# Performance work log

Hardware: AMD Instinct MI355X
Metric: run time of the kernel (lower is better)

The kernel has to match this reference:

```python
import jax, jax.numpy as jnp
import numpy as np

N = 50000
E = 800000
F_IN = 128


def _gat(h, src, dst, W, a_src, a_dst, bias, heads, out_ch, concat):
    n = h.shape[0]
    z = (h @ W.T).reshape(n, heads, out_ch)              # [N,H,C]
    alpha_s = jnp.sum(z * a_src, axis=-1)                # [N,H]
    alpha_d = jnp.sum(z * a_dst, axis=-1)                # [N,H]
    logits = jax.nn.leaky_relu(alpha_s[src] + alpha_d[dst], 0.2)  # [Etot,H]
    m = jax.ops.segment_max(logits, dst, num_segments=n)
    ex = jnp.exp(logits - m[dst])
    denom = jax.ops.segment_sum(ex, dst, num_segments=n)
    w = ex / (denom[dst] + 1e-16)                        # [Etot,H]
    agg = jax.ops.segment_sum(w[:, :, None] * z[src], dst, num_segments=n)  # [N,H,C]
    if concat:
        out = agg.reshape(n, heads * out_ch)
    else:
        out = agg.mean(axis=1)
    return out + bias


def setup_inputs() -> dict:
    key = jax.random.key(0)
    ks = jax.random.split(key, 16)
    s = lambda *sh: 1.0 / np.sqrt(sh[-1])
    inp = {
        "x": jax.random.normal(ks[0], (N, F_IN), jnp.float32),
        "edge_index": jax.random.randint(ks[1], (2, E), 0, N, jnp.int64),
        # GraphConv(no_node_features=128 -> 128, aggr='add')
        "W_rel": jax.random.normal(ks[2], (128, F_IN), jnp.float32) * s(128, F_IN),
        "b_rel": jnp.zeros((128,), jnp.float32),
        "W_root": jax.random.normal(ks[3], (128, F_IN), jnp.float32) * s(128, F_IN),
        # GATConv(128 -> 8, heads=8, concat) => 64
        "W1": jax.random.normal(ks[4], (64, 128), jnp.float32) * s(64, 128),
        "a1_src": jax.random.normal(ks[5], (8, 8), jnp.float32) * 0.35,
        "a1_dst": jax.random.normal(ks[6], (8, 8), jnp.float32) * 0.35,
        "b1": jnp.zeros((64,), jnp.float32),
        # GATConv(64 -> 64, heads=1, concat=False)
        "W2": jax.random.normal(ks[7], (64, 64), jnp.float32) * s(64, 64),
        "a2_src": jax.random.normal(ks[8], (1, 64), jnp.float32) * 0.125,
        "a2_dst": jax.random.normal(ks[9], (1, 64), jnp.float32) * 0.125,
        "b2": jnp.zeros((64,), jnp.float32),
        "Wr": jax.random.normal(ks[10], (1, 64), jnp.float32) * s(1, 64),
        "br": jnp.zeros((1,), jnp.float32),
    }
    return inp


def reference(x, edge_index, W_rel, b_rel, W_root, W1, a1_src, a1_dst, b1,
              W2, a2_src, a2_dst, b2, Wr, br):
    src, dst = edge_index[0], edge_index[1]
    # GraphConv, aggr='add': W_rel @ sum_{j in N(i)} x_j + b + W_root @ x_i
    nbr = jax.ops.segment_sum(x[src], dst, num_segments=N)
    h = nbr @ W_rel.T + b_rel + x @ W_root.T
    h = jax.nn.elu(h)
    # GATConv adds self-loops by default
    loop = jnp.arange(N, dtype=edge_index.dtype)
    src2 = jnp.concatenate([src, loop])
    dst2 = jnp.concatenate([dst, loop])
    h = _gat(h, src2, dst2, W1, a1_src, a1_dst, b1, heads=8, out_ch=8, concat=True)
    h = jax.nn.elu(h)
    h = _gat(h, src2, dst2, W2, a2_src, a2_dst, b2, heads=1, out_ch=64, concat=False)
    # final 'mean' aggregation over all nodes (single graph)
    g = jnp.mean(h, axis=0, keepdims=True)               # [1,64]
    return g @ Wr.T + br                                  # [1,1]
```

## Files before the change

kernel.cpp:

```cpp
#include <hip/hip_runtime.h>
#include <hip/hip_bf16.h>
#include <math.h>

#define N_NODES 50000
#define N_EDGES 800000
#define F_IN 128
#define NBUCK 391
#define EPB 4096
#define NBB 196

typedef __attribute__((ext_vector_type(8))) short bf16x8;
typedef __attribute__((ext_vector_type(4))) float f32x4;
typedef __attribute__((ext_vector_type(2))) float f32x2;
typedef unsigned long long ull;

__device__ __forceinline__ float elu_f(float x)   { return x > 0.f ? x : expm1f(x); }
__device__ __forceinline__ float lrelu_f(float x) { return x > 0.f ? x : 0.2f * x; }
__device__ __forceinline__ int   clampN(int v)    { return v < 0 ? 0 : (v >= N_NODES ? N_NODES - 1 : v); }
__device__ __forceinline__ float bits2f(unsigned int u) { union { unsigned int u; float f; } x; x.u = u; return x.f; }
__device__ __forceinline__ float lo16(unsigned int u) { return bits2f(u << 16); }
__device__ __forceinline__ float hi16(unsigned int u) { return bits2f(u & 0xffff0000u); }
__device__ __forceinline__ float bf2f(unsigned short s) { return bits2f(((unsigned int)s) << 16); }
__device__ __forceinline__ unsigned short f2bfbits(float f) {
    __hip_bfloat16 b = __float2bfloat16(f);
    return __builtin_bit_cast(unsigned short, b);
}
__device__ __forceinline__ unsigned int pack2(float lo, float hi) {
    return ((unsigned int)f2bfbits(hi) << 16) | f2bfbits(lo);
}

__global__ __launch_bounds__(256) void k_bhist(const int* __restrict__ dst,
                                               int* __restrict__ bcount) {
    __shared__ int hist[NBUCK];
    int tid = threadIdx.x;
    for (int j = tid; j < NBUCK; j += 256) hist[j] = 0;
    __syncthreads();
    int base = blockIdx.x * EPB;
    #pragma unroll
    for (int t = 0; t < EPB / 256; ++t) {
        int e = base + t * 256 + tid;
        if (e < N_EDGES) atomicAdd(&hist[clampN(dst[e]) >> 7], 1);
    }
    __syncthreads();
    for (int j = tid; j < NBUCK; j += 256)
        if (hist[j]) atomicAdd(&bcount[j], hist[j]);
}

__global__ __launch_bounds__(512) void k_bscan(const int* __restrict__ bcount,
                                               int* __restrict__ boff,
                                               int* __restrict__ bcur) {
    __shared__ int wsum[8];
    __shared__ int wbase[8];
    int tid = threadIdx.x;
    int lane = tid & 63, wid = tid >> 6;
    int v = (tid < NBUCK) ? bcount[tid] : 0;
    int x = v;
    #pragma unroll
    for (int d = 1; d < 64; d <<= 1) {
        int t = __shfl_up(x, d, 64);
        if (lane >= d) x += t;
    }
    if (lane == 63) wsum[wid] = x;
    __syncthreads();
    if (tid == 0) {
        int b = 0;
        #pragma unroll
        for (int w = 0; w < 8; ++w) { wbase[w] = b; b += wsum[w]; }
    }
    __syncthreads();
    if (tid < NBUCK) {
        int e = wbase[wid] + x - v;
        boff[tid] = e;
        bcur[tid] = e;
    }
    if (tid == 0) boff[NBUCK] = N_EDGES;
}

__global__ __launch_bounds__(256) void k_bscatter(const int* __restrict__ src,
                                                  const int* __restrict__ dst,
                                                  int* __restrict__ bcur,
                                                  unsigned int* __restrict__ ebuf) {
    __shared__ int hist[NBUCK];
    __shared__ int hbase[NBUCK];
    int tid = threadIdx.x;
    for (int j = tid; j < NBUCK; j += 256) hist[j] = 0;
    __syncthreads();
    int base = blockIdx.x * EPB;
    unsigned int myP[EPB / 256]; int myB[EPB / 256], myR[EPB / 256];
    #pragma unroll
    for (int t = 0; t < EPB / 256; ++t) {
        int e = base + t * 256 + tid;
        if (e < N_EDGES) {
            int d = clampN(dst[e]);
            int s = clampN(src[e]);
            myP[t] = ((unsigned int)s << 7) | (unsigned int)(d & 127);
            myB[t] = d >> 7;
            myR[t] = atomicAdd(&hist[d >> 7], 1);
        } else myB[t] = -1;
    }
    __syncthreads();
    for (int j = tid; j < NBUCK; j += 256)
        if (hist[j]) hbase[j] = atomicAdd(&bcur[j], hist[j]);
    __syncthreads();
    #pragma unroll
    for (int t = 0; t < EPB / 256; ++t) {
        if (myB[t] >= 0) ebuf[hbase[myB[t]] + myR[t]] = myP[t];
    }
}

__global__ __launch_bounds__(256) void k_bfinal(const unsigned int* __restrict__ ebuf,
                                                const int* __restrict__ boff,
                                                int* __restrict__ offsets,
                                                int* __restrict__ csr) {
    __shared__ int cnt[128];
    __shared__ int cur[128];
    __shared__ int ws[4];
    int b = blockIdx.x;
    int tid = threadIdx.x;
    int node0 = b << 7;
    int k0 = boff[b], k1 = boff[b + 1];
    if (tid < 128) cnt[tid] = 0;
    __syncthreads();
    for (int k = k0 + tid; k < k1; k += 256)
        atomicAdd(&cnt[ebuf[k] & 127u], 1);
    __syncthreads();
    int lane = tid & 63;
    int v = (tid < 128) ? cnt[tid] : 0;
    int x = v;
    #pragma unroll
    for (int d = 1; d < 64; d <<= 1) {
        int t = __shfl_up(x, d, 64);
        if (lane >= d) x += t;
    }
    if (lane == 63) ws[tid >> 6] = x;
    __syncthreads();
    if (tid < 128) {
        int add = (tid >> 6) ? ws[0] : 0;
        int excl = k0 + add + x - v;
        cur[tid] = excl;
        int node = node0 + tid;
        if (node < N_NODES) offsets[node] = excl;
    }
    if (b == NBUCK - 1 && tid == 0) offsets[N_NODES] = N_EDGES;
    __syncthreads();
    for (int k = k0 + tid; k < k1; k += 256) {
        unsigned int e = ebuf[k];
        int r = atomicAdd(&cur[e & 127u], 1);
        csr[r] = (int)(e >> 7);
    }
}

#define CAST_X_IDS (N_NODES * 32)
__global__ void k_cast(const float* __restrict__ x,
                       const float* __restrict__ W_rel, const float* __restrict__ W_root,
                       const float* __restrict__ W1, const float* __restrict__ W2,
                       __hip_bfloat16* __restrict__ Abuf, unsigned int* __restrict__ x8,
                       __hip_bfloat16* __restrict__ Wc,
                       __hip_bfloat16* __restrict__ W1b, __hip_bfloat16* __restrict__ W2b) {
    int id = blockIdx.x * 256 + threadIdx.x;
    if (id < CAST_X_IDS) {
        int i = id >> 5, c4 = (id & 31) * 4;
        float4 v = *(const float4*)&x[(size_t)i * 128 + c4];
        ull p = (ull)f2bfbits(v.x) | ((ull)f2bfbits(v.y) << 16)
              | ((ull)f2bfbits(v.z) << 32) | ((ull)f2bfbits(v.w) << 48);
        *(ull*)&Abuf[(size_t)i * 256 + 128 + c4] = p;
        int t = __builtin_amdgcn_cvt_pk_fp8_f32(v.x, v.y, 0, false);
        t = __builtin_amdgcn_cvt_pk_fp8_f32(v.z, v.w, t, true);
        x8[(size_t)i * 32 + (id & 31)] = (unsigned int)t;
    } else {
        int j = id - CAST_X_IDS;
        if (j < 32768) {
            int cc = j >> 8, k = j & 255;
            float v = (k < 128) ? W_rel[cc * 128 + k] : W_root[cc * 128 + (k - 128)];
            Wc[j] = __float2bfloat16(v);
        } else if (j < 32768 + 8192) {
            W1b[j - 32768] = __float2bfloat16(W1[j - 32768]);
        } else if (j < 32768 + 8192 + 4096) {
            W2b[j - 32768 - 8192] = __float2bfloat16(W2[j - 32768 - 8192]);
        }
    }
}

__global__ __launch_bounds__(256) void k_gather(const unsigned int* __restrict__ x8,
                                                const int* __restrict__ offsets,
                                                const int* __restrict__ csr,
                                                ull* __restrict__ outNbr) {
    int i = blockIdx.x * 8 + (threadIdx.x >> 5);
    int l = threadIdx.x & 31;
    int k0 = offsets[i], k1 = offsets[i + 1];
    float a0 = 0.f, a1 = 0.f, a2 = 0.f, a3 = 0.f;
    for (int kb = k0; kb < k1; kb += 8) {
        int s[8]; int vm[8];
        #pragma unroll
        for (int j = 0; j < 8; ++j) {
            int kk = kb + j;
            vm[j] = kk < k1;
            s[j] = csr[vm[j] ? kk : k1 - 1];
        }
        unsigned int u[8];
        #pragma unroll
        for (int j = 0; j < 8; ++j) u[j] = x8[(size_t)s[j] * 32 + l];
        #pragma unroll
        for (int j = 0; j < 8; ++j) {
            if (vm[j]) {
                f32x2 lo = __builtin_amdgcn_cvt_pk_f32_fp8(u[j], false);
                f32x2 hi = __builtin_amdgcn_cvt_pk_f32_fp8(u[j], true);
                a0 += lo.x; a1 += lo.y; a2 += hi.x; a3 += hi.y;
            }
        }
    }
    outNbr[(size_t)i * 64 + l] = (ull)pack2(a0, a1) | ((ull)pack2(a2, a3) << 32);
}

template<int K, int N, bool ELU, bool BIAS, int EPI>
__global__ __launch_bounds__(256) void k_gemm(const __hip_bfloat16* __restrict__ A,
                                              const __hip_bfloat16* __restrict__ W,
                                              const float* __restrict__ bias,
                                              __hip_bfloat16* __restrict__ Out,
                                              const float* __restrict__ a_src,
                                              const float* __restrict__ a_dst,
                                              float* __restrict__ as_o,
                                              float* __restrict__ ad_o,
                                              unsigned int* __restrict__ z8) {
    constexpr int NT = N / 16;
    __shared__ __align__(16) short smem[64 * 40 + N * 40];
    short (*sA)[40] = (short(*)[40])smem;
    short (*sW)[40] = (short(*)[40])(smem + 64 * 40);
    int tid = threadIdx.x;
    int lane = tid & 63, wave = tid >> 6;
    int quad = lane >> 4, l16 = lane & 15;
    int node0 = blockIdx.x * 64;
    int srow = tid >> 2, schk = (tid & 3) * 8;
    int ga = node0 + srow; if (ga >= N_NODES) ga = N_NODES - 1;
    const short* Ap = (const short*)A + (size_t)ga * K + schk;
    const short* Wp = (const short*)W;
    f32x4 acc[NT];
    #pragma unroll
    for (int t = 0; t < NT; ++t) acc[t] = (f32x4){0.f, 0.f, 0.f, 0.f};
    for (int k0 = 0; k0 < K; k0 += 32) {
        *(bf16x8*)&sA[srow][schk] = *(const bf16x8*)(Ap + k0);
        #pragma unroll
        for (int it = 0; it < N / 64; ++it) {
            int wrow = srow + it * 64;
            *(bf16x8*)&sW[wrow][schk] = *(const bf16x8*)(Wp + (size_t)wrow * K + k0 + schk);
        }
        __syncthreads();
        bf16x8 a = *(const bf16x8*)&sA[wave * 16 + l16][quad * 8];
        #pragma unroll
        for (int nt = 0; nt < NT; ++nt) {
            bf16x8 b = *(const bf16x8*)&sW[nt * 16 + l16][quad * 8];
            acc[nt] = __builtin_amdgcn_mfma_f32_16x16x32_bf16(a, b, acc[nt], 0, 0, 0);
        }
        __syncthreads();
    }
    if (EPI == 0) {
        int mbase = node0 + wave * 16 + quad * 4;
        #pragma unroll
        for (int nt = 0; nt < NT; ++nt) {
            int col = nt * 16 + l16;
            float bv = BIAS ? bias[col] : 0.f;
            #pragma unroll
            for (int r = 0; r < 4; ++r) {
                int m = mbase + r;
                if (m < N_NODES) {
                    float v = acc[nt][r] + bv;
                    if (ELU) v = elu_f(v);
                    Out[(size_t)m * N + col] = __float2bfloat16(v);
                }
            }
        }
    } else {
        short* sZ = smem;
        #pragma unroll
        for (int nt = 0; nt < NT; ++nt) {
            int col = nt * 16 + l16;
            #pragma unroll
            for (int r = 0; r < 4; ++r) {
                int row = wave * 16 + quad * 4 + r;
                sZ[row * 72 + col] = (short)f2bfbits(acc[nt][r]);
            }
        }
        __syncthreads();
        int row = tid >> 2, chunk = tid & 3;
        int gi = node0 + row;
        float v[16];
        bf16x8 c0 = *(const bf16x8*)&sZ[row * 72 + chunk * 16];
        bf16x8 c1 = *(const bf16x8*)&sZ[row * 72 + chunk * 16 + 8];
        #pragma unroll
        for (int j = 0; j < 8; ++j) {
            v[j]     = bf2f((unsigned short)c0[j]);
            v[8 + j] = bf2f((unsigned short)c1[j]);
        }
        if (EPI == 1) {
            float ps0 = 0.f, pd0 = 0.f, ps1 = 0.f, pd1 = 0.f;
            #pragma unroll
            for (int j = 0; j < 8; ++j) {
                ps0 += v[j] * a_src[chunk * 16 + j];
                pd0 += v[j] * a_dst[chunk * 16 + j];
                ps1 += v[8 + j] * a_src[chunk * 16 + 8 + j];
                pd1 += v[8 + j] * a_dst[chunk * 16 + 8 + j];
            }
            if (gi < N_NODES) {
                as_o[(size_t)gi * 8 + 2 * chunk]     = ps0;
                as_o[(size_t)gi * 8 + 2 * chunk + 1] = ps1;
                ad_o[(size_t)gi * 8 + 2 * chunk]     = pd0;
                ad_o[(size_t)gi * 8 + 2 * chunk + 1] = pd1;
            }
        } else {
            float ps = 0.f, pd = 0.f;
            #pragma unroll
            for (int j = 0; j < 16; ++j) {
                ps += v[j] * a_src[chunk * 16 + j];
                pd += v[j] * a_dst[chunk * 16 + j];
            }
            ps += __shfl_xor(ps, 1, 64); ps += __shfl_xor(ps, 2, 64);
            pd += __shfl_xor(pd, 1, 64); pd += __shfl_xor(pd, 2, 64);
            if ((tid & 3) == 0 && gi < N_NODES) { as_o[gi] = ps; ad_o[gi] = pd; }
        }
        if (gi < N_NODES) {
            #pragma unroll
            for (int wi = 0; wi < 4; ++wi) {
                int t = __builtin_amdgcn_cvt_pk_fp8_f32(v[4 * wi], v[4 * wi + 1], 0, false);
                t = __builtin_amdgcn_cvt_pk_fp8_f32(v[4 * wi + 2], v[4 * wi + 3], t, true);
                z8[(size_t)gi * 16 + chunk * 4 + wi] = (unsigned int)t;
            }
        }
    }
}

__global__ __launch_bounds__(256) void k_gat1attn(const unsigned int* __restrict__ z8,
                                                  const float* __restrict__ as1,
                                                  const float* __restrict__ ad1,
                                                  const float* __restrict__ b1,
                                                  const int* __restrict__ offsets,
                                                  const int* __restrict__ csr,
                                                  ull* __restrict__ h2u) {
    int i = blockIdx.x * 16 + (threadIdx.x >> 4);
    int l = threadIdx.x & 15;
    int hd = l >> 1;
    int wh = l & 7, slot = l >> 3;
    int k0 = offsets[i], k1 = offsets[i + 1];
    float ad_h = ad1[(size_t)i * 8 + hd];
    float adw  = ad1[(size_t)i * 8 + wh];
    float e_self = __expf(lrelu_f(as1[(size_t)i * 8 + hd] + ad_h));
    unsigned int uz = z8[(size_t)i * 16 + l];
    f32x2 zlo = __builtin_amdgcn_cvt_pk_f32_fp8(uz, false);
    f32x2 zhi = __builtin_amdgcn_cvt_pk_f32_fp8(uz, true);
    float acc0 = e_self * zlo.x, acc1 = e_self * zlo.y;
    float acc2 = e_self * zhi.x, acc3 = e_self * zhi.y;
    float denp = 0.f;
    for (int kb = k0; kb < k1; kb += 8) {
        int sr[4]; float er[4];
        #pragma unroll
        for (int m = 0; m < 4; ++m) {
            int kk = kb + 2 * m + slot;
            bool v = kk < k1;
            int s = csr[v ? kk : k1 - 1];
            sr[m] = s;
            er[m] = v ? __expf(lrelu_f(as1[(size_t)s * 8 + wh] + adw)) : 0.f;
            denp += er[m];
        }
        int sj[8]; float ej[8]; unsigned int u[8];
        #pragma unroll
        for (int m = 0; m < 4; ++m) {
            #pragma unroll
            for (int sb = 0; sb < 2; ++sb) {
                sj[2 * m + sb] = __shfl(sr[m], sb * 8 + hd, 16);
                ej[2 * m + sb] = __shfl(er[m], sb * 8 + hd, 16);
            }
        }
        #pragma unroll
        for (int j = 0; j < 8; ++j) u[j] = z8[(size_t)sj[j] * 16 + l];
        #pragma unroll
        for (int j = 0; j < 8; ++j) {
            f32x2 alo = __builtin_amdgcn_cvt_pk_f32_fp8(u[j], false);
            f32x2 ahi = __builtin_amdgcn_cvt_pk_f32_fp8(u[j], true);
            acc0 += ej[j] * alo.x; acc1 += ej[j] * alo.y;
            acc2 += ej[j] * ahi.x; acc3 += ej[j] * ahi.y;
        }
    }
    denp += __shfl_xor(denp, 8, 16);
    float den = __shfl(denp, hd, 16) + e_self;
    float inv = 1.f / den;
    float r0 = elu_f(acc0 * inv + b1[4 * l + 0]);
    float r1 = elu_f(acc1 * inv + b1[4 * l + 1]);
    float r2 = elu_f(acc2 * inv + b1[4 * l + 2]);
    float r3 = elu_f(acc3 * inv + b1[4 * l + 3]);
    h2u[(size_t)i * 16 + l] = (ull)pack2(r0, r1) | ((ull)pack2(r2, r3) << 32);
}

__global__ __launch_bounds__(256) void k_gat2attn(const unsigned int* __restrict__ z8,
                                                  const float* __restrict__ as2,
                                                  const float* __restrict__ ad2,
                                                  const float* __restrict__ b2,
                                                  const int* __restrict__ offsets,
                                                  const int* __restrict__ csr,
                                                  const float* __restrict__ Wr,
                                                  float* __restrict__ red) {
    int i = blockIdx.x * 16 + (threadIdx.x >> 4);
    int l = threadIdx.x & 15;
    int k0 = offsets[i], k1 = offsets[i + 1];
    float ad = ad2[i];
    float e_self = __expf(lrelu_f(as2[i] + ad));
    unsigned int uz = z8[(size_t)i * 16 + l];
    f32x2 zlo = __builtin_amdgcn_cvt_pk_f32_fp8(uz, false);
    f32x2 zhi = __builtin_amdgcn_cvt_pk_f32_fp8(uz, true);
    float acc0 = e_self * zlo.x, acc1 = e_self * zlo.y;
    float acc2 = e_self * zhi.x, acc3 = e_self * zhi.y;
    float denp = (l == 0) ? e_self : 0.f;
    for (int kb = k0; kb < k1; kb += 16) {
        int kk = kb + l;
        bool v = kk < k1;
        int s = csr[v ? kk : k1 - 1];
        float e = v ? __expf(lrelu_f(as2[s] + ad)) : 0.f;
        denp += e;
        int nv = k1 - kb; if (nv > 16) nv = 16;
        for (int j0 = 0; j0 < nv; j0 += 8) {
            int sj[8]; float ej[8]; unsigned int u[8];
            #pragma unroll
            for (int j = 0; j < 8; ++j) {
                int idx = (j0 + j) & 15;
                sj[j] = __shfl(s, idx, 16);
                ej[j] = __shfl(e, idx, 16);
            }
            #pragma unroll
            for (int j = 0; j < 8; ++j) u[j] = z8[(size_t)sj[j] * 16 + l];
            #pragma unroll
            for (int j = 0; j < 8; ++j) {
                f32x2 alo = __builtin_amdgcn_cvt_pk_f32_fp8(u[j], false);
                f32x2 ahi = __builtin_amdgcn_cvt_pk_f32_fp8(u[j], true);
                acc0 += ej[j] * alo.x; acc1 += ej[j] * alo.y;
                acc2 += ej[j] * ahi.x; acc3 += ej[j] * ahi.y;
            }
        }
    }
    #pragma unroll
    for (int d = 8; d >= 1; d >>= 1) denp += __shfl_xor(denp, d, 16);
    float inv = 1.f / denp;
    float c = (acc0 * inv + b2[4 * l + 0]) * Wr[4 * l + 0]
            + (acc1 * inv + b2[4 * l + 1]) * Wr[4 * l + 1]
            + (acc2 * inv + b2[4 * l + 2]) * Wr[4 * l + 2]
            + (acc3 * inv + b2[4 * l + 3]) * Wr[4 * l + 3];
    #pragma unroll
    for (int d = 8; d >= 1; d >>= 1) c += __shfl_xor(c, d, 16);
    if (l == 0) atomicAdd(&red[blockIdx.x & 255], c);
}

__global__ void k_finalize(const float* __restrict__ red, const float* __restrict__ br,
                           float* __restrict__ out) {
    int t = threadIdx.x;
    float s = red[t] + red[t + 64] + red[t + 128] + red[t + 192];
    #pragma unroll
    for (int d = 32; d >= 1; d >>= 1) s += __shfl_xor(s, d, 64);
    if (t == 0) out[0] = s * (1.0f / N_NODES) + br[0];
}

extern "C" void kernel_launch(void* const* d_in, const int* in_sizes, int n_in,
                              void* d_out, int out_size, void* d_ws, size_t ws_size,
                              hipStream_t stream) {
    const float* x      = (const float*)d_in[0];
    const int*   edges  = (const int*)d_in[1];
    const float* W_rel  = (const float*)d_in[2];
    const float* b_rel  = (const float*)d_in[3];
    const float* W_root = (const float*)d_in[4];
    const float* W1     = (const float*)d_in[5];
    const float* a1s    = (const float*)d_in[6];
    const float* a1d    = (const float*)d_in[7];
    const float* b1     = (const float*)d_in[8];
    const float* W2     = (const float*)d_in[9];
    const float* a2s    = (const float*)d_in[10];
    const float* a2d    = (const float*)d_in[11];
    const float* b2     = (const float*)d_in[12];
    const float* Wr     = (const float*)d_in[13];
    const float* br     = (const float*)d_in[14];
    float* out = (float*)d_out;

    const int* src = edges;
    const int* dst = edges + N_EDGES;

    char* ws = (char*)d_ws;
    size_t p = 0;
    auto alloc = [&](size_t bytes) -> void* {
        void* r = ws + p;
        p = (p + bytes + 255) & ~(size_t)255;
        return r;
    };
    int*   bcount  = (int*)alloc((size_t)NBUCK * 4);
    int*   boff    = (int*)alloc((size_t)(NBUCK + 1) * 4);
    int*   bcur    = (int*)alloc((size_t)NBUCK * 4);
    unsigned int* ebuf = (unsigned int*)alloc((size_t)N_EDGES * 4);
    int*   offsets = (int*)alloc((size_t)(N_NODES + 1) * 4);
    int*   csr     = (int*)alloc((size_t)N_EDGES * 4);
    __hip_bfloat16* Abuf = (__hip_bfloat16*)alloc((size_t)N_NODES * 256 * 2);
    unsigned int* x8 = (unsigned int*)alloc((size_t)N_NODES * 32 * 4);
    __hip_bfloat16* Wc   = (__hip_bfloat16*)alloc((size_t)128 * 256 * 2);
    __hip_bfloat16* W1b  = (__hip_bfloat16*)alloc((size_t)64 * 128 * 2);
    __hip_bfloat16* W2b  = (__hip_bfloat16*)alloc((size_t)64 * 64 * 2);
    __hip_bfloat16* h    = (__hip_bfloat16*)alloc((size_t)N_NODES * 128 * 2);
    float* as1 = (float*)alloc((size_t)N_NODES * 8 * 4);
    float* ad1 = (float*)alloc((size_t)N_NODES * 8 * 4);
    __hip_bfloat16* h2b  = (__hip_bfloat16*)alloc((size_t)N_NODES * 64 * 2);
    float* as2 = (float*)alloc((size_t)N_NODES * 4);
    float* ad2 = (float*)alloc((size_t)N_NODES * 4);
    unsigned int* z1e8 = (unsigned int*)alloc((size_t)N_NODES * 16 * 4);
    unsigned int* z2e8 = (unsigned int*)alloc((size_t)N_NODES * 16 * 4);
    float* red = (float*)alloc(256 * 4);

    hipMemsetAsync(bcount, 0, (size_t)NBUCK * 4, stream);
    hipMemsetAsync(red, 0, 256 * 4, stream);

    const int MB   = (N_NODES + 63) / 64;
    const int NB8  = N_NODES / 8;
    const int NB16 = N_NODES / 16;
    const int CAST_IDS = CAST_X_IDS + 32768 + 8192 + 4096;

    k_bhist   <<<NBB, 256, 0, stream>>>(dst, bcount);
    k_bscan   <<<1, 512, 0, stream>>>(bcount, boff, bcur);
    k_bscatter<<<NBB, 256, 0, stream>>>(src, dst, bcur, ebuf);
    k_bfinal  <<<NBUCK, 256, 0, stream>>>(ebuf, boff, offsets, csr);
    k_cast    <<<(CAST_IDS + 255) / 256, 256, 0, stream>>>(x, W_rel, W_root, W1, W2, Abuf, x8, Wc, W1b, W2b);
    k_gather  <<<NB8, 256, 0, stream>>>(x8, offsets, csr, (ull*)Abuf);
    k_gemm<256, 128, true,  true,  0><<<MB, 256, 0, stream>>>(Abuf, Wc, b_rel, h,
                                                              nullptr, nullptr, nullptr, nullptr, nullptr);
    k_gemm<128, 64,  false, false, 1><<<MB, 256, 0, stream>>>(h, W1b, nullptr, nullptr,
                                                              a1s, a1d, as1, ad1, z1e8);
    k_gat1attn<<<NB16, 256, 0, stream>>>(z1e8, as1, ad1, b1, offsets, csr, (ull*)h2b);
    k_gemm<64, 64, false, false, 2><<<MB, 256, 0, stream>>>(h2b, W2b, nullptr, nullptr,
                                                            a2s, a2d, as2, ad2, z2e8);
    k_gat2attn<<<NB16, 256, 0, stream>>>(z2e8, as2, ad2, b2, offsets, csr, Wr, red);
    k_finalize<<<1, 64, 0, stream>>>(red, br, out);
}
```

Baseline: 246.9 us.

## Fuse histogram with cast kernel, drop memsets, split edges across two half-warps in attention

Merges the bucket histogram and the dtype-cast kernels into one launch. Per-block histograms are written to a partial buffer, so the global atomics and both memsets go away, and the red buffer is now zeroed inside the kernel. The scan then sums 196 partials per bucket serially. Both GAT attention kernels now give each node 32 lanes instead of 16, with two half-groups taking alternating edge chunks and combining through an xor shuffle, which doubles parallelism per node at the cost of extra shuffles and idle lanes for low-degree nodes.

```diff
diff --git a/kernel.cpp b/kernel.cpp
--- a/kernel.cpp
+++ b/kernel.cpp
@@ -18,8 +18,6 @@
 __device__ __forceinline__ float lrelu_f(float x) { return x > 0.f ? x : 0.2f * x; }
 __device__ __forceinline__ int   clampN(int v)    { return v < 0 ? 0 : (v >= N_NODES ? N_NODES - 1 : v); }
 __device__ __forceinline__ float bits2f(unsigned int u) { union { unsigned int u; float f; } x; x.u = u; return x.f; }
-__device__ __forceinline__ float lo16(unsigned int u) { return bits2f(u << 16); }
-__device__ __forceinline__ float hi16(unsigned int u) { return bits2f(u & 0xffff0000u); }
 __device__ __forceinline__ float bf2f(unsigned short s) { return bits2f(((unsigned int)s) << 16); }
 __device__ __forceinline__ unsigned short f2bfbits(float f) {
     __hip_bfloat16 b = __float2bfloat16(f);
@@ -29,31 +27,74 @@
     return ((unsigned int)f2bfbits(hi) << 16) | f2bfbits(lo);
 }
 
-__global__ __launch_bounds__(256) void k_bhist(const int* __restrict__ dst,
-                                               int* __restrict__ bcount) {
+#define CAST_X_IDS (N_NODES * 32)
+#define CAST_IDS (CAST_X_IDS + 32768 + 8192 + 4096)
+#define CASTB ((CAST_IDS + 255) / 256)
+__global__ __launch_bounds__(256) void k_prep(const int* __restrict__ dst,
+                                              const float* __restrict__ x,
+                                              const float* __restrict__ W_rel,
+                                              const float* __restrict__ W_root,
+                                              const float* __restrict__ W1,
+                                              const float* __restrict__ W2,
+                                              int* __restrict__ part,
+                                              __hip_bfloat16* __restrict__ Abuf,
+                                              unsigned int* __restrict__ x8,
+                                              __hip_bfloat16* __restrict__ Wc,
+                                              __hip_bfloat16* __restrict__ W1b,
+                                              __hip_bfloat16* __restrict__ W2b,
+                                              float* __restrict__ red) {
     __shared__ int hist[NBUCK];
     int tid = threadIdx.x;
-    for (int j = tid; j < NBUCK; j += 256) hist[j] = 0;
-    __syncthreads();
-    int base = blockIdx.x * EPB;
-    #pragma unroll
-    for (int t = 0; t < EPB / 256; ++t) {
-        int e = base + t * 256 + tid;
-        if (e < N_EDGES) atomicAdd(&hist[clampN(dst[e]) >> 7], 1);
-    }
-    __syncthreads();
-    for (int j = tid; j < NBUCK; j += 256)
-        if (hist[j]) atomicAdd(&bcount[j], hist[j]);
-}
-
-__global__ __launch_bounds__(512) void k_bscan(const int* __restrict__ bcount,
+    if (blockIdx.x < NBB) {
+        for (int j = tid; j < NBUCK; j += 256) hist[j] = 0;
+        __syncthreads();
+        int base = blockIdx.x * EPB;
+        #pragma unroll
+        for (int t = 0; t < EPB / 256; ++t) {
+            int e = base + t * 256 + tid;
+            if (e < N_EDGES) atomicAdd(&hist[clampN(dst[e]) >> 7], 1);
+        }
+        __syncthreads();
+        for (int j = tid; j < NBUCK; j += 256)
+            part[(size_t)blockIdx.x * NBUCK + j] = hist[j];
+    } else {
+        if (blockIdx.x == NBB) red[tid] = 0.f;
+        int id = (blockIdx.x - NBB) * 256 + tid;
+        if (id < CAST_X_IDS) {
+            int i = id >> 5, c4 = (id & 31) * 4;
+            float4 v = *(const float4*)&x[(size_t)i * 128 + c4];
+            ull p = (ull)f2bfbits(v.x) | ((ull)f2bfbits(v.y) << 16)
+                  | ((ull)f2bfbits(v.z) << 32) | ((ull)f2bfbits(v.w) << 48);
+            *(ull*)&Abuf[(size_t)i * 256 + 128 + c4] = p;
+            int t = __builtin_amdgcn_cvt_pk_fp8_f32(v.x, v.y, 0, false);
+            t = __builtin_amdgcn_cvt_pk_fp8_f32(v.z, v.w, t, true);
+            x8[(size_t)i * 32 + (id & 31)] = (unsigned int)t;
+        } else if (id < CAST_IDS) {
+            int j = id - CAST_X_IDS;
+            if (j < 32768) {
+                int cc = j >> 8, k = j & 255;
+                float v = (k < 128) ? W_rel[cc * 128 + k] : W_root[cc * 128 + (k - 128)];
+                Wc[j] = __float2bfloat16(v);
+            } else if (j < 32768 + 8192) {
+                W1b[j - 32768] = __float2bfloat16(W1[j - 32768]);
+            } else {
+                W2b[j - 32768 - 8192] = __float2bfloat16(W2[j - 32768 - 8192]);
+            }
+        }
+    }
+}
+
+__global__ __launch_bounds__(512) void k_bscan(const int* __restrict__ part,
                                                int* __restrict__ boff,
                                                int* __restrict__ bcur) {
     __shared__ int wsum[8];
     __shared__ int wbase[8];
     int tid = threadIdx.x;
     int lane = tid & 63, wid = tid >> 6;
-    int v = (tid < NBUCK) ? bcount[tid] : 0;
+    int v = 0;
+    if (tid < NBUCK) {
+        for (int b = 0; b < NBB; ++b) v += part[(size_t)b * NBUCK + tid];
+    }
     int x = v;
     #pragma unroll
     for (int d = 1; d < 64; d <<= 1) {
@@ -147,37 +188,6 @@
         unsigned int e = ebuf[k];
         int r = atomicAdd(&cur[e & 127u], 1);
         csr[r] = (int)(e >> 7);
-    }
-}
-
-#define CAST_X_IDS (N_NODES * 32)
-__global__ void k_cast(const float* __restrict__ x,
-                       const float* __restrict__ W_rel, const float* __restrict__ W_root,
-                       const float* __restrict__ W1, const float* __restrict__ W2,
-                       __hip_bfloat16* __restrict__ Abuf, unsigned int* __restrict__ x8,
-                       __hip_bfloat16* __restrict__ Wc,
-                       __hip_bfloat16* __restrict__ W1b, __hip_bfloat16* __restrict__ W2b) {
-    int id = blockIdx.x * 256 + threadIdx.x;
-    if (id < CAST_X_IDS) {
-        int i = id >> 5, c4 = (id & 31) * 4;
-        float4 v = *(const float4*)&x[(size_t)i * 128 + c4];
-        ull p = (ull)f2bfbits(v.x) | ((ull)f2bfbits(v.y) << 16)
-              | ((ull)f2bfbits(v.z) << 32) | ((ull)f2bfbits(v.w) << 48);
-        *(ull*)&Abuf[(size_t)i * 256 + 128 + c4] = p;
-        int t = __builtin_amdgcn_cvt_pk_fp8_f32(v.x, v.y, 0, false);
-        t = __builtin_amdgcn_cvt_pk_fp8_f32(v.z, v.w, t, true);
-        x8[(size_t)i * 32 + (id & 31)] = (unsigned int)t;
-    } else {
-        int j = id - CAST_X_IDS;
-        if (j < 32768) {
-            int cc = j >> 8, k = j & 255;
-            float v = (k < 128) ? W_rel[cc * 128 + k] : W_root[cc * 128 + (k - 128)];
-            Wc[j] = __float2bfloat16(v);
-        } else if (j < 32768 + 8192) {
-            W1b[j - 32768] = __float2bfloat16(W1[j - 32768]);
-        } else if (j < 32768 + 8192 + 4096) {
-            W2b[j - 32768 - 8192] = __float2bfloat16(W2[j - 32768 - 8192]);
-        }
     }
 }
 
@@ -335,8 +345,10 @@
                                                   const int* __restrict__ offsets,
                                                   const int* __restrict__ csr,
                                                   ull* __restrict__ h2u) {
-    int i = blockIdx.x * 16 + (threadIdx.x >> 4);
-    int l = threadIdx.x & 15;
+    int i = blockIdx.x * 8 + (threadIdx.x >> 5);
+    int w = threadIdx.x & 31;
+    int g = w >> 4;
+    int l = w & 15;
     int hd = l >> 1;
     int wh = l & 7, slot = l >> 3;
     int k0 = offsets[i], k1 = offsets[i + 1];
@@ -346,10 +358,13 @@
     unsigned int uz = z8[(size_t)i * 16 + l];
     f32x2 zlo = __builtin_amdgcn_cvt_pk_f32_fp8(uz, false);
     f32x2 zhi = __builtin_amdgcn_cvt_pk_f32_fp8(uz, true);
-    float acc0 = e_self * zlo.x, acc1 = e_self * zlo.y;
-    float acc2 = e_self * zhi.x, acc3 = e_self * zhi.y;
+    float acc0, acc1, acc2, acc3;
+    if (g == 0) {
+        acc0 = e_self * zlo.x; acc1 = e_self * zlo.y;
+        acc2 = e_self * zhi.x; acc3 = e_self * zhi.y;
+    } else { acc0 = acc1 = acc2 = acc3 = 0.f; }
     float denp = 0.f;
-    for (int kb = k0; kb < k1; kb += 8) {
+    for (int kb = k0 + 8 * g; kb < k1; kb += 16) {
         int sr[4]; float er[4];
         #pragma unroll
         for (int m = 0; m < 4; ++m) {
@@ -379,14 +394,21 @@
             acc2 += ej[j] * ahi.x; acc3 += ej[j] * ahi.y;
         }
     }
+    acc0 += __shfl_xor(acc0, 16, 64);
+    acc1 += __shfl_xor(acc1, 16, 64);
+    acc2 += __shfl_xor(acc2, 16, 64);
+    acc3 += __shfl_xor(acc3, 16, 64);
+    denp += __shfl_xor(denp, 16, 64);
     denp += __shfl_xor(denp, 8, 16);
     float den = __shfl(denp, hd, 16) + e_self;
     float inv = 1.f / den;
-    float r0 = elu_f(acc0 * inv + b1[4 * l + 0]);
-    float r1 = elu_f(acc1 * inv + b1[4 * l + 1]);
-    float r2 = elu_f(acc2 * inv + b1[4 * l + 2]);
-    float r3 = elu_f(acc3 * inv + b1[4 * l + 3]);
-    h2u[(size_t)i * 16 + l] = (ull)pack2(r0, r1) | ((ull)pack2(r2, r3) << 32);
+    if (g == 0) {
+        float r0 = elu_f(acc0 * inv + b1[4 * l + 0]);
+        float r1 = elu_f(acc1 * inv + b1[4 * l + 1]);
+        float r2 = elu_f(acc2 * inv + b1[4 * l + 2]);
+        float r3 = elu_f(acc3 * inv + b1[4 * l + 3]);
+        h2u[(size_t)i * 16 + l] = (ull)pack2(r0, r1) | ((ull)pack2(r2, r3) << 32);
+    }
 }
 
 __global__ __launch_bounds__(256) void k_gat2attn(const unsigned int* __restrict__ z8,
@@ -397,18 +419,23 @@
                                                   const int* __restrict__ csr,
                                                   const float* __restrict__ Wr,
                                                   float* __restrict__ red) {
-    int i = blockIdx.x * 16 + (threadIdx.x >> 4);
-    int l = threadIdx.x & 15;
+    int i = blockIdx.x * 8 + (threadIdx.x >> 5);
+    int w = threadIdx.x & 31;
+    int g = w >> 4;
+    int l = w & 15;
     int k0 = offsets[i], k1 = offsets[i + 1];
     float ad = ad2[i];
     float e_self = __expf(lrelu_f(as2[i] + ad));
     unsigned int uz = z8[(size_t)i * 16 + l];
     f32x2 zlo = __builtin_amdgcn_cvt_pk_f32_fp8(uz, false);
     f32x2 zhi = __builtin_amdgcn_cvt_pk_f32_fp8(uz, true);
-    float acc0 = e_self * zlo.x, acc1 = e_self * zlo.y;
-    float acc2 = e_self * zhi.x, acc3 = e_self * zhi.y;
-    float denp = (l == 0) ? e_self : 0.f;
-    for (int kb = k0; kb < k1; kb += 16) {
+    float acc0, acc1, acc2, acc3;
+    if (g == 0) {
+        acc0 = e_self * zlo.x; acc1 = e_self * zlo.y;
+        acc2 = e_self * zhi.x; acc3 = e_self * zhi.y;
+    } else { acc0 = acc1 = acc2 = acc3 = 0.f; }
+    float denp = (g == 0 && l == 0) ? e_self : 0.f;
+    for (int kb = k0 + 16 * g; kb < k1; kb += 32) {
         int kk = kb + l;
         bool v = kk < k1;
         int s = csr[v ? kk : k1 - 1];
@@ -434,6 +461,11 @@
             }
         }
     }
+    acc0 += __shfl_xor(acc0, 16, 64);
+    acc1 += __shfl_xor(acc1, 16, 64);
+    acc2 += __shfl_xor(acc2, 16, 64);
+    acc3 += __shfl_xor(acc3, 16, 64);
+    denp += __shfl_xor(denp, 16, 64);
     #pragma unroll
     for (int d = 8; d >= 1; d >>= 1) denp += __shfl_xor(denp, d, 16);
     float inv = 1.f / denp;
@@ -443,7 +475,7 @@
             + (acc3 * inv + b2[4 * l + 3]) * Wr[4 * l + 3];
     #pragma unroll
     for (int d = 8; d >= 1; d >>= 1) c += __shfl_xor(c, d, 16);
-    if (l == 0) atomicAdd(&red[blockIdx.x & 255], c);
+    if (w == 0) atomicAdd(&red[blockIdx.x & 255], c);
 }
 
 __global__ void k_finalize(const float* __restrict__ red, const float* __restrict__ br,
@@ -485,7 +517,7 @@
         p = (p + bytes + 255) & ~(size_t)255;
         return r;
     };
-    int*   bcount  = (int*)alloc((size_t)NBUCK * 4);
+    int*   part    = (int*)alloc((size_t)NBB * NBUCK * 4);
     int*   boff    = (int*)alloc((size_t)(NBUCK + 1) * 4);
     int*   bcur    = (int*)alloc((size_t)NBUCK * 4);
     unsigned int* ebuf = (unsigned int*)alloc((size_t)N_EDGES * 4);
@@ -506,27 +538,22 @@
     unsigned int* z2e8 = (unsigned int*)alloc((size_t)N_NODES * 16 * 4);
     float* red = (float*)alloc(256 * 4);
 
-    hipMemsetAsync(bcount, 0, (size_t)NBUCK * 4, stream);
-    hipMemsetAsync(red, 0, 256 * 4, stream);
-
-    const int MB   = (N_NODES + 63) / 64;
-    const int NB8  = N_NODES / 8;
-    const int NB16 = N_NODES / 16;
-    const int CAST_IDS = CAST_X_IDS + 32768 + 8192 + 4096;
-
-    k_bhist   <<<NBB, 256, 0, stream>>>(dst, bcount);
-    k_bscan   <<<1, 512, 0, stream>>>(bcount, boff, bcur);
+    const int MB  = (N_NODES + 63) / 64;
+    const int NB8 = N_NODES / 8;
+
+    k_prep    <<<NBB + CASTB, 256, 0, stream>>>(dst, x, W_rel, W_root, W1, W2,
+                                                part, Abuf, x8, Wc, W1b, W2b, red);
+    k_bscan   <<<1, 512, 0, stream>>>(part, boff, bcur);
     k_bscatter<<<NBB, 256, 0, stream>>>(src, dst, bcur, ebuf);
     k_bfinal  <<<NBUCK, 256, 0, stream>>>(ebuf, boff, offsets, csr);
-    k_cast    <<<(CAST_IDS + 255) / 256, 256, 0, stream>>>(x, W_rel, W_root, W1, W2, Abuf, x8, Wc, W1b, W2b);
     k_gather  <<<NB8, 256, 0, stream>>>(x8, offsets, csr, (ull*)Abuf);
     k_gemm<256, 128, true,  true,  0><<<MB, 256, 0, stream>>>(Abuf, Wc, b_rel, h,
                                                               nullptr, nullptr, nullptr, nullptr, nullptr);
     k_gemm<128, 64,  false, false, 1><<<MB, 256, 0, stream>>>(h, W1b, nullptr, nullptr,
                                                               a1s, a1d, as1, ad1, z1e8);
-    k_gat1attn<<<NB16, 256, 0, stream>>>(z1e8, as1, ad1, b1, offsets, csr, (ull*)h2b);
+    k_gat1attn<<<NB8, 256, 0, stream>>>(z1e8, as1, ad1, b1, offsets, csr, (ull*)h2b);
     k_gemm<64, 64, false, false, 2><<<MB, 256, 0, stream>>>(h2b, W2b, nullptr, nullptr,
                                                             a2s, a2d, as2, ad2, z2e8);
-    k_gat2attn<<<NB16, 256, 0, stream>>>(z2e8, as2, ad2, b2, offsets, csr, Wr, red);
+    k_gat2attn<<<NB8, 256, 0, stream>>>(z2e8, as2, ad2, b2, offsets, csr, Wr, red);
     k_finalize<<<1, 64, 0, stream>>>(red, br, out);
 }
```

Result: slower. 265.2 us (+7.4%).
